# Kernel optimization log

Hardware: AMD Instinct MI355X
Metric: run time of the kernel (lower is better)

Reference implementation:

```python
import jax, jax.numpy as jnp
import numpy as np

B, N, D, L = 4, 256, 512, 3  # batch, seq_len, input_dim, n_layer


def setup_inputs() -> dict:
    key = jax.random.key(0)
    ks = jax.random.split(key, 12)
    s = 0.02
    return {
        "x": jax.random.normal(ks[0], (B, N, D), dtype=jnp.float32),
        # Highway: L layers, each a gate Linear(D,D) and transform Linear(D,D)
        "hw_gate_w": jax.random.normal(ks[1], (L, D, D), dtype=jnp.float32) * s,
        "hw_gate_b": jnp.zeros((L, D), dtype=jnp.float32),
        "hw_tr_w": jax.random.normal(ks[2], (L, D, D), dtype=jnp.float32) * s,
        "hw_tr_b": jnp.zeros((L, D), dtype=jnp.float32),
        # link_weight MLP: Linear(2D,D) -> ReLU -> [Linear(D,D) -> ReLU]*(L-2) -> Linear(D,1) -> Sigmoid
        "lw0_w": jax.random.normal(ks[3], (D, 2 * D), dtype=jnp.float32) * s,
        "lw0_b": jnp.zeros((D,), dtype=jnp.float32),
        "lw1_w": jax.random.normal(ks[4], (D, D), dtype=jnp.float32) * s,
        "lw1_b": jnp.zeros((D,), dtype=jnp.float32),
        "lwo_w": jax.random.normal(ks[5], (1, D), dtype=jnp.float32) * s,
        "lwo_b": jnp.zeros((1,), dtype=jnp.float32),
    }


def _highway(x, gw, gb, tw, tb):
    # standard highway: y = g * relu(Wt x + bt) + (1 - g) * x, g = sigmoid(Wg x + bg)
    for i in range(gw.shape[0]):
        g = jax.nn.sigmoid(jnp.einsum('bnd,ed->bne', x, gw[i]) + gb[i])
        t = jax.nn.relu(jnp.einsum('bnd,ed->bne', x, tw[i]) + tb[i])
        x = g * t + (1.0 - g) * x
    return x


def reference(x, hw_gate_w, hw_gate_b, hw_tr_w, hw_tr_b,
              lw0_w, lw0_b, lw1_w, lw1_b, lwo_w, lwo_b):
    d = x.shape[-1]
    h = _highway(x, hw_gate_w, hw_gate_b, hw_tr_w, hw_tr_b)  # [B,N,D]
    # Fused pairwise-concat + first Linear: cat(h_i, h_j) @ W0.T ==
    # h_i @ W0[:, :D].T + h_j @ W0[:, D:].T  (avoids the [B,N*N,2D] tensor)
    a = jnp.einsum('bnd,ed->bne', h, lw0_w[:, :d])  # uses m1 (row i)
    b = jnp.einsum('bnd,ed->bne', h, lw0_w[:, d:])  # uses m2 (col j)
    z = jax.nn.relu(a[:, :, None, :] + b[:, None, :, :] + lw0_b)  # [B,N,N,D]
    # (dropout is identity in eval mode)
    z = jax.nn.relu(jnp.einsum('bijd,ed->bije', z, lw1_w) + lw1_b)  # n_layer-2 == 1 hidden layer
    out = jax.nn.sigmoid(jnp.einsum('bijd,d->bij', z, lwo_w[0]) + lwo_b[0])
    return out  # [B,N,N]
```

## Files before the change

### kernel.cpp

```cpp
#include <hip/hip_runtime.h>
#include <hip/hip_bf16.h>

#define BB 4
#define NN 256
#define DD 512

using short8   = __attribute__((ext_vector_type(8))) short;
using f32x4    = __attribute__((ext_vector_type(4))) float;
using uint32x4 = __attribute__((ext_vector_type(4))) unsigned int;

__device__ __forceinline__ unsigned short f2bf(float f) {
    unsigned int u = __float_as_uint(f);
    unsigned int r = (u + 0x7fffu + ((u >> 16) & 1u)) >> 16;
    return (unsigned short)r;
}

__device__ __forceinline__ unsigned cvtpk(float lo, float hi) {
    unsigned r;
    asm("v_cvt_pk_bf16_f32 %0, %1, %2" : "=v"(r) : "v"(lo), "v"(hi));
    return r;
}

template <int ROWS, int NW>
__device__ __forceinline__ void stage_rows(const unsigned short* src, int stride,
                                           short* dst, int tid) {
    int wave = tid >> 6, lane = tid & 63;
#pragma unroll
    for (int c = 0; c < ROWS / (8 * NW); ++c) {
        int rbase = (c * NW + wave) * 8;
        int row   = rbase + (lane >> 3);
        int slot  = (lane & 7) ^ (row & 7);
        const unsigned short* g = src + (size_t)row * stride + slot * 8;
        __builtin_amdgcn_global_load_lds(
            (const __attribute__((address_space(1))) void*)g,
            (__attribute__((address_space(3))) void*)(dst + rbase * 64),
            16, 0, 0);
    }
}

__device__ __forceinline__ short8 read_frag(const short* T, int rowBase, int k2) {
    int lane = threadIdx.x & 63;
    int row  = rowBase + (lane & 15);
    int slot = ((k2 * 4) + (lane >> 4)) ^ (row & 7);
    return *(const short8*)(T + row * 64 + slot * 8);
}

__global__ void prep_kernel(const float* __restrict__ x,
                            const float* __restrict__ gw, const float* __restrict__ tw,
                            const float* __restrict__ w0, const float* __restrict__ w1,
                            float* __restrict__ h0_f32, unsigned short* __restrict__ h0_bf,
                            unsigned short* __restrict__ wg_bf, unsigned short* __restrict__ wt_bf,
                            unsigned short* __restrict__ w0c_bf, unsigned short* __restrict__ w1_bf) {
    const int S_X = BB * NN * DD;
    const int S_W = 3 * DD * DD;
    const int S_W0 = 2 * DD * DD;
    const int S_W1 = DD * DD;
    int total = S_X + S_W + S_W + S_W0 + S_W1;
    for (int idx = blockIdx.x * blockDim.x + threadIdx.x; idx < total;
         idx += gridDim.x * blockDim.x) {
        int t = idx;
        if (t < S_X) { float v = x[t]; h0_f32[t] = v; h0_bf[t] = f2bf(v); continue; }
        t -= S_X;
        if (t < S_W) { wg_bf[t] = f2bf(gw[t]); continue; }
        t -= S_W;
        if (t < S_W) { wt_bf[t] = f2bf(tw[t]); continue; }
        t -= S_W;
        if (t < S_W0) {
            int e = t >> 9, d = t & 511;
            float v = (e < DD) ? w0[e * (2 * DD) + d] : w0[(e - DD) * (2 * DD) + DD + d];
            w0c_bf[t] = f2bf(v); continue;
        }
        t -= S_W0;
        w1_bf[t] = f2bf(w1[t]);
    }
}

__global__ __launch_bounds__(256) void highway_kernel(
        const float* __restrict__ h_in, const unsigned short* __restrict__ hbf_in,
        const unsigned short* __restrict__ wg_bf, const unsigned short* __restrict__ wt_bf,
        const float* __restrict__ gb, const float* __restrict__ tb,
        float* __restrict__ h_out, unsigned short* __restrict__ hbf_out) {
    __shared__ short ht[64 * 64];
    __shared__ short wgt[64 * 64];
    __shared__ short wtt[64 * 64];
    int tid = threadIdx.x, lane = tid & 63, wave = tid >> 6;
    int mt = blockIdx.x >> 3, et = blockIdx.x & 7;
    int m0 = mt * 64, e0 = et * 64;
    int wm = wave >> 1, we = wave & 1;
    f32x4 gacc[2][2] = {}, tacc[2][2] = {};
    for (int ks = 0; ks < 8; ++ks) {
        int d0 = ks * 64;
        __syncthreads();
        stage_rows<64, 4>(hbf_in + (size_t)m0 * DD + d0, DD, ht, tid);
        stage_rows<64, 4>(wg_bf + (size_t)e0 * DD + d0, DD, wgt, tid);
        stage_rows<64, 4>(wt_bf + (size_t)e0 * DD + d0, DD, wtt, tid);
        __syncthreads();
#pragma unroll
        for (int k2 = 0; k2 < 2; ++k2) {
            short8 af[2], bg[2], bt[2];
#pragma unroll
            for (int f = 0; f < 2; ++f) af[f] = read_frag(ht, wm * 32 + f * 16, k2);
#pragma unroll
            for (int f = 0; f < 2; ++f) bg[f] = read_frag(wgt, we * 32 + f * 16, k2);
#pragma unroll
            for (int f = 0; f < 2; ++f) bt[f] = read_frag(wtt, we * 32 + f * 16, k2);
#pragma unroll
            for (int fm = 0; fm < 2; ++fm)
#pragma unroll
                for (int fn = 0; fn < 2; ++fn) {
                    gacc[fm][fn] = __builtin_amdgcn_mfma_f32_16x16x32_bf16(af[fm], bg[fn], gacc[fm][fn], 0, 0, 0);
                    tacc[fm][fn] = __builtin_amdgcn_mfma_f32_16x16x32_bf16(af[fm], bt[fn], tacc[fm][fn], 0, 0, 0);
                }
        }
    }
#pragma unroll
    for (int fm = 0; fm < 2; ++fm)
#pragma unroll
        for (int fn = 0; fn < 2; ++fn) {
            int e = e0 + we * 32 + fn * 16 + (lane & 15);
            float gbe = gb[e], tbe = tb[e];
#pragma unroll
            for (int r = 0; r < 4; ++r) {
                int m = m0 + wm * 32 + fm * 16 + (lane >> 4) * 4 + r;
                float g = 1.f / (1.f + __expf(-(gacc[fm][fn][r] + gbe)));
                float tv = tacc[fm][fn][r] + tbe; tv = tv > 0.f ? tv : 0.f;
                float ho = h_in[(size_t)m * DD + e];
                float hn = g * tv + (1.f - g) * ho;
                h_out[(size_t)m * DD + e] = hn;
                hbf_out[(size_t)m * DD + e] = f2bf(hn);
            }
        }
}

__global__ __launch_bounds__(256) void ab_kernel(
        const unsigned short* __restrict__ hbf, const unsigned short* __restrict__ w0c_bf,
        const float* __restrict__ lw0_b,
        float* __restrict__ a_out, float* __restrict__ b_out) {
    __shared__ short ht[64 * 64];
    __shared__ short wt_[128 * 64];
    int tid = threadIdx.x, lane = tid & 63, wave = tid >> 6;
    int mt = blockIdx.x >> 3, et = blockIdx.x & 7;
    int m0 = mt * 64, e0 = et * 128;
    int wm = wave >> 1, we = wave & 1;
    f32x4 acc[2][4] = {};
    for (int ks = 0; ks < 8; ++ks) {
        __syncthreads();
        stage_rows<64, 4>(hbf + (size_t)m0 * DD + ks * 64, DD, ht, tid);
        stage_rows<128, 4>(w0c_bf + (size_t)e0 * DD + ks * 64, DD, wt_, tid);
        __syncthreads();
#pragma unroll
        for (int k2 = 0; k2 < 2; ++k2) {
            short8 af[2], bf_[4];
#pragma unroll
            for (int f = 0; f < 2; ++f) af[f] = read_frag(ht, wm * 32 + f * 16, k2);
#pragma unroll
            for (int f = 0; f < 4; ++f) bf_[f] = read_frag(wt_, we * 64 + f * 16, k2);
#pragma unroll
            for (int fm = 0; fm < 2; ++fm)
#pragma unroll
                for (int fn = 0; fn < 4; ++fn)
                    acc[fm][fn] = __builtin_amdgcn_mfma_f32_16x16x32_bf16(af[fm], bf_[fn], acc[fm][fn], 0, 0, 0);
        }
    }
#pragma unroll
    for (int fm = 0; fm < 2; ++fm)
#pragma unroll
        for (int fn = 0; fn < 4; ++fn) {
            int e = e0 + we * 64 + fn * 16 + (lane & 15);
#pragma unroll
            for (int r = 0; r < 4; ++r) {
                int m = m0 + wm * 32 + fm * 16 + (lane >> 4) * 4 + r;
                float v = acc[fm][fn][r];
                if (e < DD) a_out[(size_t)m * DD + e] = v + lw0_b[e];
                else        b_out[(size_t)m * DD + (e - DD)] = v;
            }
        }
}


#define Z_LOADS(K)                                                            \
    {                                                                         \
        const int dl_ = (K) * 64 + s * 8;                                     \
        alo = *(const f32x4*)(arow + dl_);                                    \
        ahi = *(const f32x4*)(arow + dl_ + 4);                                \
        const float* b0_ = brow + (size_t)rr * DD + dl_;                      \
        const float* b1_ = brow + (size_t)(64 + rr) * DD + dl_;               \
        b0lo = *(const f32x4*)b0_; b0hi = *(const f32x4*)(b0_ + 4);           \
        b1lo = *(const f32x4*)b1_; b1hi = *(const f32x4*)(b1_ + 4);           \
    }

#define Z_MATH()                                                              \
    {                                                                         \
        zw0[0] = cvtpk(fmaxf(alo[0] + b0lo[0], 0.f), fmaxf(alo[1] + b0lo[1], 0.f)); \
        zw0[1] = cvtpk(fmaxf(alo[2] + b0lo[2], 0.f), fmaxf(alo[3] + b0lo[3], 0.f)); \
        zw0[2] = cvtpk(fmaxf(ahi[0] + b0hi[0], 0.f), fmaxf(ahi[1] + b0hi[1], 0.f)); \
        zw0[3] = cvtpk(fmaxf(ahi[2] + b0hi[2], 0.f), fmaxf(ahi[3] + b0hi[3], 0.f)); \
        zw1[0] = cvtpk(fmaxf(alo[0] + b1lo[0], 0.f), fmaxf(alo[1] + b1lo[1], 0.f)); \
        zw1[1] = cvtpk(fmaxf(alo[2] + b1lo[2], 0.f), fmaxf(alo[3] + b1lo[3], 0.f)); \
        zw1[2] = cvtpk(fmaxf(ahi[0] + b1hi[0], 0.f), fmaxf(ahi[1] + b1hi[1], 0.f)); \
        zw1[3] = cvtpk(fmaxf(ahi[2] + b1hi[2], 0.f), fmaxf(ahi[3] + b1hi[3], 0.f)); \
    }

#define Z_WRITE(BUF)                                                          \
    {                                                                         \
        *(uint32x4*)((BUF) + rr * 64 + ((s ^ (rr & 7)) * 8)) = zw0;           \
        const int r1_ = 64 + rr;                                              \
        *(uint32x4*)((BUF) + r1_ * 64 + ((s ^ (r1_ & 7)) * 8)) = zw1;         \
    }

__global__ __launch_bounds__(512, 2) void pair_kernel(
        const float* __restrict__ a_f32, const float* __restrict__ b_f32,
        const unsigned short* __restrict__ w1_bf,
        const float* __restrict__ lw1_b, const float* __restrict__ lwo_w,
        const float* __restrict__ lwo_b, float* __restrict__ out) {
    __shared__ short ws[2][512 * 64];
    __shared__ short zs[2][128 * 64];
    int tid = threadIdx.x, lane = tid & 63, wave = tid >> 6;
    int bid = blockIdx.x;
    int swz = (bid & 7) * 256 + (bid >> 3);
    int bb = swz >> 9, i = (swz >> 1) & 255, j0 = (swz & 1) * 128;
    const float* arow = a_f32 + (size_t)(bb * NN + i) * DD;
    const float* brow = b_f32 + (size_t)(bb * NN + j0) * DD;
    int s = tid & 7, rr = tid >> 3;
    int we = wave;

    f32x4 acc[8][4] = {};
    uint32x4 zw0, zw1;
    f32x4 alo, ahi, b0lo, b0hi, b1lo, b1hi;

    Z_LOADS(0)
    stage_rows<512, 8>(w1_bf, DD, ws[0], tid);
    Z_MATH()
    Z_WRITE(zs[0])
    asm volatile("s_waitcnt lgkmcnt(0)" ::: "memory");

#pragma unroll
    for (int k = 0; k < 8; ++k) {
        __builtin_amdgcn_s_barrier();
        __builtin_amdgcn_sched_barrier(0);
        if (k < 7) {
            Z_LOADS(k + 1)
            stage_rows<512, 8>(w1_bf + (size_t)(k + 1) * 64, DD, ws[(k + 1) & 1], tid);
            asm volatile("s_waitcnt vmcnt(14)" ::: "memory");
        } else {
            asm volatile("s_waitcnt vmcnt(0)" ::: "memory");
        }
        __builtin_amdgcn_sched_barrier(0);

        const short* zc = zs[k & 1];
        const short* wc = ws[k & 1];
        __builtin_amdgcn_s_setprio(1);
#pragma unroll
        for (int k2 = 0; k2 < 2; ++k2) {
            short8 bfr[4];
#pragma unroll
            for (int f = 0; f < 4; ++f) bfr[f] = read_frag(wc, we * 64 + f * 16, k2);
#pragma unroll
            for (int fh = 0; fh < 2; ++fh) {
                short8 af[4];
#pragma unroll
                for (int f = 0; f < 4; ++f) af[f] = read_frag(zc, (fh * 4 + f) * 16, k2);
#pragma unroll
                for (int fm = 0; fm < 4; ++fm)
#pragma unroll
                    for (int fn = 0; fn < 4; ++fn)
                        acc[fh * 4 + fm][fn] = __builtin_amdgcn_mfma_f32_16x16x32_bf16(
                            af[fm], bfr[fn], acc[fh * 4 + fm][fn], 0, 0, 0);
            }
        }
        __builtin_amdgcn_s_setprio(0);

        if (k < 7) {
            Z_MATH()
            Z_WRITE(zs[(k + 1) & 1])
            asm volatile("s_waitcnt lgkmcnt(0)" ::: "memory");
        }
    }

    __syncthreads();
    float* s_red = (float*)zs;
#pragma unroll
    for (int fm = 0; fm < 8; ++fm) {
        float red[4] = {0.f, 0.f, 0.f, 0.f};
#pragma unroll
        for (int fn = 0; fn < 4; ++fn) {
            int e = we * 64 + fn * 16 + (lane & 15);
            float b1e = lw1_b[e], woe = lwo_w[e];
#pragma unroll
            for (int r = 0; r < 4; ++r) {
                float v = acc[fm][fn][r] + b1e;
                red[r] += (v > 0.f) ? v * woe : 0.f;
            }
        }
#pragma unroll
        for (int mask = 1; mask < 16; mask <<= 1)
#pragma unroll
            for (int r = 0; r < 4; ++r) red[r] += __shfl_xor(red[r], mask, 64);
        if ((lane & 15) == 0) {
#pragma unroll
            for (int r = 0; r < 4; ++r)
                s_red[we * 128 + fm * 16 + (lane >> 4) * 4 + r] = red[r];
        }
    }
    __syncthreads();
    if (tid < 128) {
        float v = lwo_b[0];
#pragma unroll
        for (int w8 = 0; w8 < 8; ++w8) v += s_red[w8 * 128 + tid];
        out[((size_t)(bb * NN + i)) * NN + j0 + tid] = 1.f / (1.f + __expf(-v));
    }
}

extern "C" void kernel_launch(void* const* d_in, const int* in_sizes, int n_in,
                              void* d_out, int out_size, void* d_ws, size_t ws_size,
                              hipStream_t stream) {
    const float* x    = (const float*)d_in[0];
    const float* gw   = (const float*)d_in[1];
    const float* gb   = (const float*)d_in[2];
    const float* tw   = (const float*)d_in[3];
    const float* tb   = (const float*)d_in[4];
    const float* w0   = (const float*)d_in[5];
    const float* w0b  = (const float*)d_in[6];
    const float* w1   = (const float*)d_in[7];
    const float* w1b_ = (const float*)d_in[8];
    const float* wo   = (const float*)d_in[9];
    const float* wob  = (const float*)d_in[10];
    float* out = (float*)d_out;

    char* w = (char*)d_ws;
    float* hA  = (float*)w;            w += (size_t)BB * NN * DD * 4;
    float* hB  = (float*)w;            w += (size_t)BB * NN * DD * 4;
    unsigned short* hbA = (unsigned short*)w; w += (size_t)BB * NN * DD * 2;
    unsigned short* hbB = (unsigned short*)w; w += (size_t)BB * NN * DD * 2;
    float* a_f = (float*)w;            w += (size_t)BB * NN * DD * 4;
    float* b_f = (float*)w;            w += (size_t)BB * NN * DD * 4;
    unsigned short* wg_bf  = (unsigned short*)w; w += (size_t)3 * DD * DD * 2;
    unsigned short* wt_bf  = (unsigned short*)w; w += (size_t)3 * DD * DD * 2;
    unsigned short* w0c_bf = (unsigned short*)w; w += (size_t)2 * DD * DD * 2;
    unsigned short* w1_bf  = (unsigned short*)w; w += (size_t)DD * DD * 2;

    prep_kernel<<<1024, 256, 0, stream>>>(x, gw, tw, w0, w1, hA, hbA, wg_bf, wt_bf, w0c_bf, w1_bf);

    highway_kernel<<<128, 256, 0, stream>>>(hA, hbA, wg_bf + 0 * DD * DD, wt_bf + 0 * DD * DD,
                                            gb + 0 * DD, tb + 0 * DD, hB, hbB);
    highway_kernel<<<128, 256, 0, stream>>>(hB, hbB, wg_bf + 1 * DD * DD, wt_bf + 1 * DD * DD,
                                            gb + 1 * DD, tb + 1 * DD, hA, hbA);
    highway_kernel<<<128, 256, 0, stream>>>(hA, hbA, wg_bf + 2 * DD * DD, wt_bf + 2 * DD * DD,
                                            gb + 2 * DD, tb + 2 * DD, hB, hbB);

    ab_kernel<<<128, 256, 0, stream>>>(hbB, w0c_bf, w0b, a_f, b_f);

    pair_kernel<<<2048, 512, 0, stream>>>(a_f, b_f, w1_bf, w1b_, wo, wob, out);
}
```

Baseline: 220.3 us.

## Split pair-kernel K-step into four barrier-separated phases interleaving loads with MFMA

Restructures the main loop of the pair kernel into four sub-phases, each loading one quarter of the A/B fragments from LDS, then running one quarter of the MFMA work. Staging of the next W1 tile is split in two halves, and the z-operand global loads and math are spread across the phases. The aim is to overlap global-to-LDS traffic and elementwise z computation with matrix-core work. In exchange it adds many more workgroup barriers and full vmcnt/lgkmcnt drains per iteration, which may serialize waves.

```diff
diff --git a/kernel.cpp b/kernel.cpp
--- a/kernel.cpp
+++ b/kernel.cpp
@@ -38,6 +38,23 @@
     }
 }
 
+template <int C0, int C1>
+__device__ __forceinline__ void stage_part(const unsigned short* src, int stride,
+                                           short* dst, int tid) {
+    int wave = tid >> 6, lane = tid & 63;
+#pragma unroll
+    for (int c = C0; c < C1; ++c) {
+        int rbase = (c * 8 + wave) * 8;
+        int row   = rbase + (lane >> 3);
+        int slot  = (lane & 7) ^ (row & 7);
+        const unsigned short* g = src + (size_t)row * stride + slot * 8;
+        __builtin_amdgcn_global_load_lds(
+            (const __attribute__((address_space(1))) void*)g,
+            (__attribute__((address_space(3))) void*)(dst + rbase * 64),
+            16, 0, 0);
+    }
+}
+
 __device__ __forceinline__ short8 read_frag(const short* T, int rowBase, int k2) {
     int lane = threadIdx.x & 63;
     int row  = rowBase + (lane & 15);
@@ -54,8 +71,7 @@
     const int S_X = BB * NN * DD;
     const int S_W = 3 * DD * DD;
     const int S_W0 = 2 * DD * DD;
-    const int S_W1 = DD * DD;
-    int total = S_X + S_W + S_W + S_W0 + S_W1;
+    int total = S_X + S_W + S_W + S_W0 + DD * DD;
     for (int idx = blockIdx.x * blockDim.x + threadIdx.x; idx < total;
          idx += gridDim.x * blockDim.x) {
         int t = idx;
@@ -208,6 +224,24 @@
         *(uint32x4*)((BUF) + r1_ * 64 + ((s ^ (r1_ & 7)) * 8)) = zw1;         \
     }
 
+#define LGKM0_FENCE                                                           \
+    asm volatile("s_waitcnt lgkmcnt(0)" ::: "memory");                        \
+    __builtin_amdgcn_sched_barrier(0);
+
+#define VM0_FENCE                                                             \
+    asm volatile("s_waitcnt vmcnt(0)" ::: "memory");                          \
+    __builtin_amdgcn_sched_barrier(0);
+
+#define MFMA_Q(ABASE, BFR)                                                    \
+    __builtin_amdgcn_s_setprio(1);                                            \
+    _Pragma("unroll")                                                         \
+    for (int fm = 0; fm < 4; ++fm)                                            \
+        _Pragma("unroll")                                                     \
+        for (int fn = 0; fn < 4; ++fn)                                        \
+            acc[(ABASE) + fm][fn] = __builtin_amdgcn_mfma_f32_16x16x32_bf16(  \
+                af[fm], (BFR)[fn], acc[(ABASE) + fm][fn], 0, 0, 0);           \
+    __builtin_amdgcn_s_setprio(0);
+
 __global__ __launch_bounds__(512, 2) void pair_kernel(
         const float* __restrict__ a_f32, const float* __restrict__ b_f32,
         const unsigned short* __restrict__ w1_bf,
@@ -229,52 +263,61 @@
     f32x4 alo, ahi, b0lo, b0hi, b1lo, b1hi;
 
     Z_LOADS(0)
-    stage_rows<512, 8>(w1_bf, DD, ws[0], tid);
+    stage_part<0, 8>(w1_bf, DD, ws[0], tid);
     Z_MATH()
     Z_WRITE(zs[0])
     asm volatile("s_waitcnt lgkmcnt(0)" ::: "memory");
+    VM0_FENCE
+    __builtin_amdgcn_s_barrier();
 
 #pragma unroll
     for (int k = 0; k < 8; ++k) {
-        __builtin_amdgcn_s_barrier();
-        __builtin_amdgcn_sched_barrier(0);
-        if (k < 7) {
-            Z_LOADS(k + 1)
-            stage_rows<512, 8>(w1_bf + (size_t)(k + 1) * 64, DD, ws[(k + 1) & 1], tid);
-            asm volatile("s_waitcnt vmcnt(14)" ::: "memory");
-        } else {
-            asm volatile("s_waitcnt vmcnt(0)" ::: "memory");
-        }
-        __builtin_amdgcn_sched_barrier(0);
-
         const short* zc = zs[k & 1];
         const short* wc = ws[k & 1];
-        __builtin_amdgcn_s_setprio(1);
-#pragma unroll
-        for (int k2 = 0; k2 < 2; ++k2) {
-            short8 bfr[4];
-#pragma unroll
-            for (int f = 0; f < 4; ++f) bfr[f] = read_frag(wc, we * 64 + f * 16, k2);
-#pragma unroll
-            for (int fh = 0; fh < 2; ++fh) {
-                short8 af[4];
-#pragma unroll
-                for (int f = 0; f < 4; ++f) af[f] = read_frag(zc, (fh * 4 + f) * 16, k2);
-#pragma unroll
-                for (int fm = 0; fm < 4; ++fm)
-#pragma unroll
-                    for (int fn = 0; fn < 4; ++fn)
-                        acc[fh * 4 + fm][fn] = __builtin_amdgcn_mfma_f32_16x16x32_bf16(
-                            af[fm], bfr[fn], acc[fh * 4 + fm][fn], 0, 0, 0);
-            }
-        }
-        __builtin_amdgcn_s_setprio(0);
-
+        short8 af[4], bfr0[4], bfr1[4];
+
+#pragma unroll
+        for (int f = 0; f < 4; ++f) bfr0[f] = read_frag(wc, we * 64 + f * 16, 0);
+#pragma unroll
+        for (int f = 0; f < 4; ++f) af[f] = read_frag(zc, f * 16, 0);
+        if (k < 7) stage_part<0, 4>(w1_bf + (size_t)(k + 1) * 64, DD,
+                                    ws[(k + 1) & 1], tid);
+        __builtin_amdgcn_s_barrier();
+        LGKM0_FENCE
+        MFMA_Q(0, bfr0)
+        __builtin_amdgcn_s_barrier();
+
+#pragma unroll
+        for (int f = 0; f < 4; ++f) af[f] = read_frag(zc, 64 + f * 16, 0);
+        if (k < 7) {
+            stage_part<4, 8>(w1_bf + (size_t)(k + 1) * 64, DD, ws[(k + 1) & 1], tid);
+            Z_LOADS(k + 1)
+        }
+        __builtin_amdgcn_s_barrier();
+        LGKM0_FENCE
+        MFMA_Q(4, bfr0)
+        __builtin_amdgcn_s_barrier();
+
+#pragma unroll
+        for (int f = 0; f < 4; ++f) bfr1[f] = read_frag(wc, we * 64 + f * 16, 1);
+#pragma unroll
+        for (int f = 0; f < 4; ++f) af[f] = read_frag(zc, f * 16, 1);
+        __builtin_amdgcn_s_barrier();
+        LGKM0_FENCE
+        MFMA_Q(0, bfr1)
         if (k < 7) {
             Z_MATH()
             Z_WRITE(zs[(k + 1) & 1])
-            asm volatile("s_waitcnt lgkmcnt(0)" ::: "memory");
-        }
+        }
+        __builtin_amdgcn_s_barrier();
+
+#pragma unroll
+        for (int f = 0; f < 4; ++f) af[f] = read_frag(zc, 64 + f * 16, 1);
+        __builtin_amdgcn_s_barrier();
+        LGKM0_FENCE
+        MFMA_Q(4, bfr1)
+        VM0_FENCE
+        __builtin_amdgcn_s_barrier();
     }
 
     __syncthreads();
```

New measurement: 221.8 us. About the same (+0.7%).

## Split pair kernel across 16 waves with 2x8 wave tiling over rows and columns

Applied to the files above, without the earlier changes.

The pair kernel now launches 1024 threads per block instead of 512. Waves are arranged as a 2x8 grid, so each wave computes a 64x64 output tile with a 4x4 accumulator array instead of 128x64 with 8x4. Each thread builds one z row chunk per k step, and the prefetch/wait scheme is simplified to a full vmcnt(0) wait plus a barrier at the end of each step. The intent is higher occupancy and lower register pressure, which should help latency hiding. The trade-off is that each wave reads more LDS per MFMA, and the stricter synchronisation may stall more.

```diff
diff --git a/kernel.cpp b/kernel.cpp
--- a/kernel.cpp
+++ b/kernel.cpp
@@ -54,8 +54,7 @@
     const int S_X = BB * NN * DD;
     const int S_W = 3 * DD * DD;
     const int S_W0 = 2 * DD * DD;
-    const int S_W1 = DD * DD;
-    int total = S_X + S_W + S_W + S_W0 + S_W1;
+    int total = S_X + S_W + S_W + S_W0 + DD * DD;
     for (int idx = blockIdx.x * blockDim.x + threadIdx.x; idx < total;
          idx += gridDim.x * blockDim.x) {
         int t = idx;
@@ -177,38 +176,15 @@
         }
 }
 
-
-#define Z_LOADS(K)                                                            \
-    {                                                                         \
-        const int dl_ = (K) * 64 + s * 8;                                     \
-        alo = *(const f32x4*)(arow + dl_);                                    \
-        ahi = *(const f32x4*)(arow + dl_ + 4);                                \
-        const float* b0_ = brow + (size_t)rr * DD + dl_;                      \
-        const float* b1_ = brow + (size_t)(64 + rr) * DD + dl_;               \
-        b0lo = *(const f32x4*)b0_; b0hi = *(const f32x4*)(b0_ + 4);           \
-        b1lo = *(const f32x4*)b1_; b1hi = *(const f32x4*)(b1_ + 4);           \
-    }
-
-#define Z_MATH()                                                              \
-    {                                                                         \
-        zw0[0] = cvtpk(fmaxf(alo[0] + b0lo[0], 0.f), fmaxf(alo[1] + b0lo[1], 0.f)); \
-        zw0[1] = cvtpk(fmaxf(alo[2] + b0lo[2], 0.f), fmaxf(alo[3] + b0lo[3], 0.f)); \
-        zw0[2] = cvtpk(fmaxf(ahi[0] + b0hi[0], 0.f), fmaxf(ahi[1] + b0hi[1], 0.f)); \
-        zw0[3] = cvtpk(fmaxf(ahi[2] + b0hi[2], 0.f), fmaxf(ahi[3] + b0hi[3], 0.f)); \
-        zw1[0] = cvtpk(fmaxf(alo[0] + b1lo[0], 0.f), fmaxf(alo[1] + b1lo[1], 0.f)); \
-        zw1[1] = cvtpk(fmaxf(alo[2] + b1lo[2], 0.f), fmaxf(alo[3] + b1lo[3], 0.f)); \
-        zw1[2] = cvtpk(fmaxf(ahi[0] + b1hi[0], 0.f), fmaxf(ahi[1] + b1hi[1], 0.f)); \
-        zw1[3] = cvtpk(fmaxf(ahi[2] + b1hi[2], 0.f), fmaxf(ahi[3] + b1hi[3], 0.f)); \
-    }
-
-#define Z_WRITE(BUF)                                                          \
-    {                                                                         \
-        *(uint32x4*)((BUF) + rr * 64 + ((s ^ (rr & 7)) * 8)) = zw0;           \
-        const int r1_ = 64 + rr;                                              \
-        *(uint32x4*)((BUF) + r1_ * 64 + ((s ^ (r1_ & 7)) * 8)) = zw1;         \
-    }
-
-__global__ __launch_bounds__(512, 2) void pair_kernel(
+#define LGKM0_FENCE                                                           \
+    asm volatile("s_waitcnt lgkmcnt(0)" ::: "memory");                        \
+    __builtin_amdgcn_sched_barrier(0);
+
+#define VM0_FENCE                                                             \
+    asm volatile("s_waitcnt vmcnt(0)" ::: "memory");                          \
+    __builtin_amdgcn_sched_barrier(0);
+
+__global__ __launch_bounds__(1024, 4) void pair_kernel(
         const float* __restrict__ a_f32, const float* __restrict__ b_f32,
         const unsigned short* __restrict__ w1_bf,
         const float* __restrict__ lw1_b, const float* __restrict__ lwo_w,
@@ -222,65 +198,82 @@
     const float* arow = a_f32 + (size_t)(bb * NN + i) * DD;
     const float* brow = b_f32 + (size_t)(bb * NN + j0) * DD;
     int s = tid & 7, rr = tid >> 3;
-    int we = wave;
-
-    f32x4 acc[8][4] = {};
-    uint32x4 zw0, zw1;
-    f32x4 alo, ahi, b0lo, b0hi, b1lo, b1hi;
-
-    Z_LOADS(0)
-    stage_rows<512, 8>(w1_bf, DD, ws[0], tid);
-    Z_MATH()
-    Z_WRITE(zs[0])
+    int wm = wave >> 3, we = wave & 7;
+
+    f32x4 acc[4][4] = {};
+    f32x4 alo, ahi, blo, bhi;
+
+    {
+        const float* bp = brow + (size_t)rr * DD + s * 8;
+        alo = *(const f32x4*)(arow + s * 8);
+        ahi = *(const f32x4*)(arow + s * 8 + 4);
+        blo = *(const f32x4*)bp;
+        bhi = *(const f32x4*)(bp + 4);
+    }
+    stage_rows<512, 16>(w1_bf, DD, ws[0], tid);
+    {
+        uint32x4 zw;
+        zw[0] = cvtpk(fmaxf(alo[0] + blo[0], 0.f), fmaxf(alo[1] + blo[1], 0.f));
+        zw[1] = cvtpk(fmaxf(alo[2] + blo[2], 0.f), fmaxf(alo[3] + blo[3], 0.f));
+        zw[2] = cvtpk(fmaxf(ahi[0] + bhi[0], 0.f), fmaxf(ahi[1] + bhi[1], 0.f));
+        zw[3] = cvtpk(fmaxf(ahi[2] + bhi[2], 0.f), fmaxf(ahi[3] + bhi[3], 0.f));
+        *(uint32x4*)(zs[0] + rr * 64 + ((s ^ (rr & 7)) * 8)) = zw;
+    }
     asm volatile("s_waitcnt lgkmcnt(0)" ::: "memory");
+    VM0_FENCE
+    __builtin_amdgcn_s_barrier();
 
 #pragma unroll
     for (int k = 0; k < 8; ++k) {
-        __builtin_amdgcn_s_barrier();
-        __builtin_amdgcn_sched_barrier(0);
-        if (k < 7) {
-            Z_LOADS(k + 1)
-            stage_rows<512, 8>(w1_bf + (size_t)(k + 1) * 64, DD, ws[(k + 1) & 1], tid);
-            asm volatile("s_waitcnt vmcnt(14)" ::: "memory");
-        } else {
-            asm volatile("s_waitcnt vmcnt(0)" ::: "memory");
-        }
-        __builtin_amdgcn_sched_barrier(0);
-
         const short* zc = zs[k & 1];
         const short* wc = ws[k & 1];
-        __builtin_amdgcn_s_setprio(1);
+
+        if (k < 7) {
+            stage_rows<512, 16>(w1_bf + (size_t)(k + 1) * 64, DD,
+                                ws[(k + 1) & 1], tid);
+            const int d0 = (k + 1) * 64 + s * 8;
+            const float* bp = brow + (size_t)rr * DD + d0;
+            alo = *(const f32x4*)(arow + d0);
+            ahi = *(const f32x4*)(arow + d0 + 4);
+            blo = *(const f32x4*)bp;
+            bhi = *(const f32x4*)(bp + 4);
+        }
+
 #pragma unroll
         for (int k2 = 0; k2 < 2; ++k2) {
-            short8 bfr[4];
+            short8 af[4], bfr[4];
+#pragma unroll
+            for (int f = 0; f < 4; ++f) af[f]  = read_frag(zc, wm * 64 + f * 16, k2);
 #pragma unroll
             for (int f = 0; f < 4; ++f) bfr[f] = read_frag(wc, we * 64 + f * 16, k2);
-#pragma unroll
-            for (int fh = 0; fh < 2; ++fh) {
-                short8 af[4];
-#pragma unroll
-                for (int f = 0; f < 4; ++f) af[f] = read_frag(zc, (fh * 4 + f) * 16, k2);
-#pragma unroll
-                for (int fm = 0; fm < 4; ++fm)
-#pragma unroll
-                    for (int fn = 0; fn < 4; ++fn)
-                        acc[fh * 4 + fm][fn] = __builtin_amdgcn_mfma_f32_16x16x32_bf16(
-                            af[fm], bfr[fn], acc[fh * 4 + fm][fn], 0, 0, 0);
-            }
-        }
-        __builtin_amdgcn_s_setprio(0);
+            LGKM0_FENCE
+            __builtin_amdgcn_s_setprio(1);
+#pragma unroll
+            for (int fm = 0; fm < 4; ++fm)
+#pragma unroll
+                for (int fn = 0; fn < 4; ++fn)
+                    acc[fm][fn] = __builtin_amdgcn_mfma_f32_16x16x32_bf16(
+                        af[fm], bfr[fn], acc[fm][fn], 0, 0, 0);
+            __builtin_amdgcn_s_setprio(0);
+        }
 
         if (k < 7) {
-            Z_MATH()
-            Z_WRITE(zs[(k + 1) & 1])
+            uint32x4 zw;
+            zw[0] = cvtpk(fmaxf(alo[0] + blo[0], 0.f), fmaxf(alo[1] + blo[1], 0.f));
+            zw[1] = cvtpk(fmaxf(alo[2] + blo[2], 0.f), fmaxf(alo[3] + blo[3], 0.f));
+            zw[2] = cvtpk(fmaxf(ahi[0] + bhi[0], 0.f), fmaxf(ahi[1] + bhi[1], 0.f));
+            zw[3] = cvtpk(fmaxf(ahi[2] + bhi[2], 0.f), fmaxf(ahi[3] + bhi[3], 0.f));
+            *(uint32x4*)(zs[(k + 1) & 1] + rr * 64 + ((s ^ (rr & 7)) * 8)) = zw;
             asm volatile("s_waitcnt lgkmcnt(0)" ::: "memory");
         }
+        VM0_FENCE
+        __builtin_amdgcn_s_barrier();
     }
 
     __syncthreads();
     float* s_red = (float*)zs;
 #pragma unroll
-    for (int fm = 0; fm < 8; ++fm) {
+    for (int fm = 0; fm < 4; ++fm) {
         float red[4] = {0.f, 0.f, 0.f, 0.f};
 #pragma unroll
         for (int fn = 0; fn < 4; ++fn) {
@@ -299,7 +292,7 @@
         if ((lane & 15) == 0) {
 #pragma unroll
             for (int r = 0; r < 4; ++r)
-                s_red[we * 128 + fm * 16 + (lane >> 4) * 4 + r] = red[r];
+                s_red[we * 128 + wm * 64 + fm * 16 + (lane >> 4) * 4 + r] = red[r];
         }
     }
     __syncthreads();
@@ -350,5 +343,5 @@
 
     ab_kernel<<<128, 256, 0, stream>>>(hbB, w0c_bf, w0b, a_f, b_f);
 
-    pair_kernel<<<2048, 512, 0, stream>>>(a_f, b_f, w1_bf, w1b_, wo, wob, out);
-}
+    pair_kernel<<<2048, 1024, 0, stream>>>(a_f, b_f, w1_bf, w1b_, wo, wob, out);
+}
```

Measured after the change: 339.2 us. 1.54x slower.

## Load W1 MFMA fragments directly from global memory instead of LDS staging

Applied to the files above, without the earlier changes.

Drops the double-buffered LDS staging of the W1 weight tile in the pair kernel. Each wave now reads its B fragments straight from global memory (expected to be L2/cache resident) and switches to a 2x4 wave grid, so each wave covers 64 rows by 128 output columns. This removes 128KB of LDS traffic and writes per block, frees LDS for higher occupancy, and drops the per-step global-to-LDS copy. In exchange the kernel takes on global-load latency inside the MFMA loop, with no explicit prefetch, and redundant W1 reads across waves and blocks.

```diff
diff --git a/kernel.cpp b/kernel.cpp
--- a/kernel.cpp
+++ b/kernel.cpp
@@ -54,8 +54,7 @@
     const int S_X = BB * NN * DD;
     const int S_W = 3 * DD * DD;
     const int S_W0 = 2 * DD * DD;
-    const int S_W1 = DD * DD;
-    int total = S_X + S_W + S_W + S_W0 + S_W1;
+    int total = S_X + S_W + S_W + S_W0 + DD * DD;
     for (int idx = blockIdx.x * blockDim.x + threadIdx.x; idx < total;
          idx += gridDim.x * blockDim.x) {
         int t = idx;
@@ -213,7 +212,6 @@
         const unsigned short* __restrict__ w1_bf,
         const float* __restrict__ lw1_b, const float* __restrict__ lwo_w,
         const float* __restrict__ lwo_b, float* __restrict__ out) {
-    __shared__ short ws[2][512 * 64];
     __shared__ short zs[2][128 * 64];
     int tid = threadIdx.x, lane = tid & 63, wave = tid >> 6;
     int bid = blockIdx.x;
@@ -222,69 +220,62 @@
     const float* arow = a_f32 + (size_t)(bb * NN + i) * DD;
     const float* brow = b_f32 + (size_t)(bb * NN + j0) * DD;
     int s = tid & 7, rr = tid >> 3;
-    int we = wave;
-
-    f32x4 acc[8][4] = {};
+    int wm = wave >> 2, we = wave & 3;
+
+    const unsigned short* wsl = w1_bf + (size_t)(we * 128 + (lane & 15)) * DD
+                                       + (lane >> 4) * 8;
+
+    f32x4 acc[4][8] = {};
     uint32x4 zw0, zw1;
     f32x4 alo, ahi, b0lo, b0hi, b1lo, b1hi;
 
     Z_LOADS(0)
-    stage_rows<512, 8>(w1_bf, DD, ws[0], tid);
     Z_MATH()
     Z_WRITE(zs[0])
     asm volatile("s_waitcnt lgkmcnt(0)" ::: "memory");
+    __builtin_amdgcn_s_barrier();
 
 #pragma unroll
     for (int k = 0; k < 8; ++k) {
-        __builtin_amdgcn_s_barrier();
-        __builtin_amdgcn_sched_barrier(0);
-        if (k < 7) {
-            Z_LOADS(k + 1)
-            stage_rows<512, 8>(w1_bf + (size_t)(k + 1) * 64, DD, ws[(k + 1) & 1], tid);
-            asm volatile("s_waitcnt vmcnt(14)" ::: "memory");
-        } else {
-            asm volatile("s_waitcnt vmcnt(0)" ::: "memory");
-        }
-        __builtin_amdgcn_sched_barrier(0);
-
         const short* zc = zs[k & 1];
-        const short* wc = ws[k & 1];
-        __builtin_amdgcn_s_setprio(1);
+
+        if (k < 7) Z_LOADS(k + 1)
+
 #pragma unroll
         for (int k2 = 0; k2 < 2; ++k2) {
-            short8 bfr[4];
-#pragma unroll
-            for (int f = 0; f < 4; ++f) bfr[f] = read_frag(wc, we * 64 + f * 16, k2);
-#pragma unroll
-            for (int fh = 0; fh < 2; ++fh) {
-                short8 af[4];
-#pragma unroll
-                for (int f = 0; f < 4; ++f) af[f] = read_frag(zc, (fh * 4 + f) * 16, k2);
-#pragma unroll
-                for (int fm = 0; fm < 4; ++fm)
-#pragma unroll
-                    for (int fn = 0; fn < 4; ++fn)
-                        acc[fh * 4 + fm][fn] = __builtin_amdgcn_mfma_f32_16x16x32_bf16(
-                            af[fm], bfr[fn], acc[fh * 4 + fm][fn], 0, 0, 0);
-            }
-        }
-        __builtin_amdgcn_s_setprio(0);
+            short8 af[4], bfr[8];
+#pragma unroll
+            for (int f = 0; f < 4; ++f) af[f] = read_frag(zc, wm * 64 + f * 16, k2);
+#pragma unroll
+            for (int fn = 0; fn < 8; ++fn)
+                bfr[fn] = *(const short8*)(wsl + (size_t)(fn * 16) * DD +
+                                           k * 64 + k2 * 32);
+            __builtin_amdgcn_s_setprio(1);
+#pragma unroll
+            for (int fm = 0; fm < 4; ++fm)
+#pragma unroll
+                for (int fn = 0; fn < 8; ++fn)
+                    acc[fm][fn] = __builtin_amdgcn_mfma_f32_16x16x32_bf16(
+                        af[fm], bfr[fn], acc[fm][fn], 0, 0, 0);
+            __builtin_amdgcn_s_setprio(0);
+        }
 
         if (k < 7) {
             Z_MATH()
             Z_WRITE(zs[(k + 1) & 1])
             asm volatile("s_waitcnt lgkmcnt(0)" ::: "memory");
         }
+        __builtin_amdgcn_s_barrier();
     }
 
     __syncthreads();
     float* s_red = (float*)zs;
 #pragma unroll
-    for (int fm = 0; fm < 8; ++fm) {
+    for (int fm = 0; fm < 4; ++fm) {
         float red[4] = {0.f, 0.f, 0.f, 0.f};
 #pragma unroll
-        for (int fn = 0; fn < 4; ++fn) {
-            int e = we * 64 + fn * 16 + (lane & 15);
+        for (int fn = 0; fn < 8; ++fn) {
+            int e = we * 128 + fn * 16 + (lane & 15);
             float b1e = lw1_b[e], woe = lwo_w[e];
 #pragma unroll
             for (int r = 0; r < 4; ++r) {
@@ -299,14 +290,14 @@
         if ((lane & 15) == 0) {
 #pragma unroll
             for (int r = 0; r < 4; ++r)
-                s_red[we * 128 + fm * 16 + (lane >> 4) * 4 + r] = red[r];
+                s_red[we * 128 + wm * 64 + fm * 16 + (lane >> 4) * 4 + r] = red[r];
         }
     }
     __syncthreads();
     if (tid < 128) {
         float v = lwo_b[0];
 #pragma unroll
-        for (int w8 = 0; w8 < 8; ++w8) v += s_red[w8 * 128 + tid];
+        for (int w4 = 0; w4 < 4; ++w4) v += s_red[w4 * 128 + tid];
         out[((size_t)(bb * NN + i)) * NN + j0 + tid] = 1.f / (1.f + __expf(-v));
     }
 }
```

After: 366.0 us. 66.1% more time.
